# Kernel optimization log

Measured on AMD Instinct MI355X. Metric: run time of the kernel, lower is better.

The kernel has to match this reference:

```python
import jax, jax.numpy as jnp
import numpy as np

B, S, K = 4, 2048, 8
N_NEURONS, N_BASIS, RANK = 64, 32, 8
D_MODEL, D_HID = 256, 1024


def setup_inputs() -> dict:
    key = jax.random.key(0)
    ks = jax.random.split(key, 10)
    x = jax.random.normal(ks[0], (B, S, D_MODEL), dtype=jnp.float32)
    neuron_idx = jax.random.randint(ks[1], (B, S, K), 0, N_NEURONS)
    w = jax.random.uniform(ks[2], (B, S, K), dtype=jnp.float32)
    neuron_weights = w / jnp.sum(w, axis=-1, keepdims=True)  # softmax-like routing weights
    neuron_recipes = jax.random.normal(ks[3], (N_NEURONS, N_BASIS), dtype=jnp.float32) * 0.5
    sc = 0.1
    basis_A1 = jax.random.normal(ks[4], (N_BASIS, 16, RANK, 8), dtype=jnp.float32) * sc
    basis_A2 = jax.random.normal(ks[5], (N_BASIS, RANK, 16, 8), dtype=jnp.float32) * sc
    basis_B1 = jax.random.normal(ks[6], (N_BASIS, 8, RANK, 32), dtype=jnp.float32) * sc
    basis_B2 = jax.random.normal(ks[7], (N_BASIS, RANK, 8, 32), dtype=jnp.float32) * sc
    w_down_w = jax.random.normal(ks[8], (D_HID, D_MODEL), dtype=jnp.float32) * (1.0 / np.sqrt(D_HID))
    w_down_b = jnp.zeros((D_MODEL,), dtype=jnp.float32)
    return {
        "x": x, "neuron_idx": neuron_idx, "neuron_weights": neuron_weights,
        "neuron_recipes": neuron_recipes,
        "basis_A1": basis_A1, "basis_A2": basis_A2,
        "basis_B1": basis_B1, "basis_B2": basis_B2,
        "w_down_w": w_down_w, "w_down_b": w_down_b,
    }


def reference(x, neuron_idx, neuron_weights, neuron_recipes,
              basis_A1, basis_A2, basis_B1, basis_B2, w_down_w, w_down_b):
    Bt, St, D = x.shape
    # --- routing: gather recipes of selected neurons, softmax, weighted-combine ---
    sel = neuron_recipes[neuron_idx]                       # [B,S,k,n_basis]
    sel = jax.nn.softmax(sel, axis=-1)
    wr = jnp.einsum('bskn,bsk->bsn', sel, neuron_weights)  # [B,S,n_basis]
    # --- build per-token TT cores from basis banks (get_neuron_tt_cores) ---
    cA1 = jnp.einsum('bsn,nirk->bsirk', wr, basis_A1)      # [B,S,16,r,8]
    cA2 = jnp.einsum('bsn,nrjl->bsrjl', wr, basis_A2)      # [B,S,r,16,8]
    cB1 = jnp.einsum('bsn,nirk->bsirk', wr, basis_B1)      # [B,S,8,r,32]
    cB2 = jnp.einsum('bsn,nrjl->bsrjl', wr, basis_B2)      # [B,S,r,8,32]
    # --- TT FFN: 256 -> 64 ---
    x_fold = x.reshape(Bt, St, 16, 16)
    temp = jnp.einsum('bsij,bsirk->bsjrk', x_fold, cA1)
    h = jnp.einsum('bsjrk,bsrjl->bskl', temp, cA2).reshape(Bt, St, 64)
    # --- TT FFN: 64 -> 1024 ---
    h_fold = h.reshape(Bt, St, 8, 8)
    temp = jnp.einsum('bsij,bsirk->bsjrk', h_fold, cB1)
    out = jnp.einsum('bsjrk,bsrjl->bskl', temp, cB2).reshape(Bt, St, D_HID)
    out = jax.nn.gelu(out, approximate=False)              # torch F.gelu default = exact erf
    return out @ w_down_w + w_down_b                       # [B,S,256]
```

## Files before the change

### kernel.cpp

```cpp
#include <hip/hip_runtime.h>
#include <math.h>


typedef unsigned short u16;
typedef unsigned int u32;
typedef __attribute__((ext_vector_type(8))) __bf16 bf16x8;
typedef __attribute__((ext_vector_type(4))) float f32x4;
typedef __attribute__((ext_vector_type(16))) float f32x16;
union ABCast { float4 f; bf16x8 v; };
union U4Cast { u32 u[4]; bf16x8 v; };
union BFBits { __bf16 b; u16 u; };
union Pack8 { u16 u[8]; float4 f; };

__device__ __forceinline__ float gelu_exact(float v) {
    return 0.5f * v * (1.0f + erff(v * 0.70710678118654752440f));
}
__device__ __forceinline__ u16 f2bf_bits(float f) { BFBits c; c.b = (__bf16)f; return c.u; }
__device__ __forceinline__ float bfbits2f(u16 u) { BFBits c; c.u = u; return (float)c.b; }

__global__ __launch_bounds__(64) void k_route(
    const int* __restrict__ nidx, const float* __restrict__ nw,
    const float* __restrict__ recipes, float* __restrict__ wr_out,
    u16* __restrict__ wrAh, u16* __restrict__ wrAl)
{
    const int t = blockIdx.x * 64 + threadIdx.x;
    float acc[32];
#pragma unroll
    for (int n = 0; n < 32; n++) acc[n] = 0.f;
#pragma unroll
    for (int k = 0; k < 8; k++) {
        const int   id = nidx[t * 8 + k];
        const float wk = nw[t * 8 + k];
        const float4* row = (const float4*)(recipes + id * 32);
        float v[32];
#pragma unroll
        for (int q = 0; q < 8; q++) {
            float4 f = row[q];
            v[q*4+0] = f.x; v[q*4+1] = f.y; v[q*4+2] = f.z; v[q*4+3] = f.w;
        }
        float m = v[0];
#pragma unroll
        for (int n = 1; n < 32; n++) m = fmaxf(m, v[n]);
        float s = 0.f;
#pragma unroll
        for (int n = 0; n < 32; n++) { float e = expf(v[n] - m); v[n] = e; s += e; }
        const float iv = wk / s;
#pragma unroll
        for (int n = 0; n < 32; n++) acc[n] += v[n] * iv;
    }
    float4* o = (float4*)(wr_out + t * 32);
#pragma unroll
    for (int q = 0; q < 8; q++)
        o[q] = make_float4(acc[q*4+0], acc[q*4+1], acc[q*4+2], acc[q*4+3]);

    const int tg16 = t >> 4, tl = t & 15;
#pragma unroll
    for (int c = 0; c < 4; c++) {
        Pack8 ph, pl;
#pragma unroll
        for (int e = 0; e < 8; e++) {
            const float v = acc[c*8 + e];
            const u16 hb = f2bf_bits(v);
            ph.u[e] = hb;
            pl.u[e] = f2bf_bits(v - bfbits2f(hb));
        }
        const int lane = c * 16 + tl;
        *(float4*)(wrAh + (tg16*64 + lane)*8) = ph.f;
        *(float4*)(wrAl + (tg16*64 + lane)*8) = pl.f;
    }
}

__global__ __launch_bounds__(512) void k_stageA(
    const float* __restrict__ x, const float* __restrict__ wr,
    const float* __restrict__ A1, const float* __restrict__ A2,
    float* __restrict__ h_out)
{
    __shared__ float ca[8 * 1024];
    __shared__ float tl[8 * 1088];
    const int tid = threadIdx.x;
    const int t0  = blockIdx.x * 8;
    {
        const int e2 = tid * 2;
        float2 c[8];
#pragma unroll
        for (int tt = 0; tt < 8; tt++) c[tt] = make_float2(0.f, 0.f);
#pragma unroll 4
        for (int n = 0; n < 32; n++) {
            const float2 a = *(const float2*)(A1 + n * 1024 + e2);
#pragma unroll
            for (int tt = 0; tt < 8; tt++) {
                const float s = wr[(t0 + tt) * 32 + n];
                c[tt].x += s * a.x; c[tt].y += s * a.y;
            }
        }
#pragma unroll
        for (int tt = 0; tt < 8; tt++) *(float2*)(ca + tt * 1024 + e2) = c[tt];
    }
    __syncthreads();
    {
        const int t = tid >> 6, g = tid & 63, j = g >> 2, eh = g & 3;
        float xr[16];
#pragma unroll
        for (int i = 0; i < 16; i++) xr[i] = x[(t0 + t) * 256 + i * 16 + j];
        float tr[16];
#pragma unroll
        for (int q = 0; q < 16; q++) tr[q] = 0.f;
#pragma unroll
        for (int i = 0; i < 16; i++) {
            const float xv = xr[i];
#pragma unroll
            for (int q = 0; q < 4; q++) {
                const float4 cv = *(const float4*)(ca + t * 1024 + i * 64 + eh * 16 + q * 4);
                tr[q*4+0] += xv * cv.x; tr[q*4+1] += xv * cv.y;
                tr[q*4+2] += xv * cv.z; tr[q*4+3] += xv * cv.w;
            }
        }
#pragma unroll
        for (int q = 0; q < 4; q++)
            *(float4*)(tl + t * 1088 + j * 68 + eh * 16 + q * 4) =
                make_float4(tr[q*4+0], tr[q*4+1], tr[q*4+2], tr[q*4+3]);
    }
    __syncthreads();
    {
        const int e2 = tid * 2;
        float2 c[8];
#pragma unroll
        for (int tt = 0; tt < 8; tt++) c[tt] = make_float2(0.f, 0.f);
#pragma unroll 4
        for (int n = 0; n < 32; n++) {
            const float2 a = *(const float2*)(A2 + n * 1024 + e2);
#pragma unroll
            for (int tt = 0; tt < 8; tt++) {
                const float s = wr[(t0 + tt) * 32 + n];
                c[tt].x += s * a.x; c[tt].y += s * a.y;
            }
        }
#pragma unroll
        for (int tt = 0; tt < 8; tt++) *(float2*)(ca + tt * 1024 + e2) = c[tt];
    }
    __syncthreads();
    {
        const int t = tid >> 6, g = tid & 63, k = g >> 3, l = g & 7;
        float acc = 0.f;
#pragma unroll
        for (int j = 0; j < 16; j++) {
#pragma unroll
            for (int r = 0; r < 8; r++) {
                acc += tl[t * 1088 + j * 68 + r * 8 + k] *
                       ca[t * 1024 + r * 128 + j * 8 + l];
            }
        }
        h_out[(t0 + t) * 64 + g] = acc;
    }
}

__global__ __launch_bounds__(256) void k_bsplit(
    const float* __restrict__ B1, const float* __restrict__ B2,
    u16* __restrict__ o1h, u16* __restrict__ o1l,
    u16* __restrict__ o2h, u16* __restrict__ o2l)
{
    const int slot = blockIdx.x * 256 + threadIdx.x;
    const int bank = slot >> 13, r = (slot >> 10) & 7, g = (slot >> 6) & 15, l = slot & 63;
    const int c = l & 15, nb = 8 * (l >> 4);
    const int base = (bank == 0)
        ? ((g >> 1) * 256 + r * 32 + (g & 1) * 16 + c)
        : (r * 256 + (g >> 1) * 32 + (g & 1) * 16 + c);
    const float* S = (bank ? B2 : B1) + base + nb * 2048;
    Pack8 ph, pl;
#pragma unroll
    for (int e = 0; e < 8; e++) {
        const float v = S[e * 2048];
        const u16 hb = f2bf_bits(v);
        ph.u[e] = hb;
        pl.u[e] = f2bf_bits(v - bfbits2f(hb));
    }
    const int d = ((r * 16 + g) * 64 + l) * 8;
    *(float4*)((bank ? o2h : o1h) + d) = ph.f;
    *(float4*)((bank ? o2l : o1l) + d) = pl.f;
}

__global__ __launch_bounds__(256) void k_wsplit(
    const float* __restrict__ W, u16* __restrict__ wfh, u16* __restrict__ wfl)
{
    const int slot = blockIdx.x * 256 + threadIdx.x;
    const int ng = slot >> 11, kc = (slot >> 6) & 31, l = slot & 63;
    const float* S = W + (kc * 32 + 8 * (l >> 4)) * 256 + ng * 16 + (l & 15);
    Pack8 ph, pl;
#pragma unroll
    for (int e = 0; e < 8; e++) {
        const float v = S[e * 256];
        const u16 hb = f2bf_bits(v);
        ph.u[e] = hb;
        pl.u[e] = f2bf_bits(v - bfbits2f(hb));
    }
    const int d = ((ng * 32 + kc) * 64 + l) * 8;
    *(float4*)(wfh + d) = ph.f;
    *(float4*)(wfl + d) = pl.f;
}

__global__ __launch_bounds__(1024, 2) void k_fusedB(
    const float* __restrict__ hin,
    const u16* __restrict__ wrAh, const u16* __restrict__ wrAl,
    const u16* __restrict__ bf1h, const u16* __restrict__ bf1l,
    const u16* __restrict__ bf2h, const u16* __restrict__ bf2l,
    const u16* __restrict__ wfh, const u16* __restrict__ wfl,
    const float* __restrict__ bias, float* __restrict__ y)
{
    __shared__ __align__(16) unsigned char smem[65536];
    float* stg1 = (float*)smem;
    float* stg2 = stg1 + 8192;
    u16* gAh = (u16*)smem;
    u16* gAl = gAh + 16384;

    const int tid = threadIdx.x;
    const int l   = tid & 63;
    const int w   = tid >> 6;
    const int tg  = blockIdx.x;
    const int t0  = tg * 16;
    const int kP  = l & 31;
    const int jh  = l >> 5;

    float hreg[32];
#pragma unroll
    for (int i = 0; i < 8; i++)
#pragma unroll
        for (int jj = 0; jj < 4; jj++)
            hreg[i*4+jj] = hin[(t0 + w) * 64 + i * 8 + jh * 4 + jj];

    ABCast cu;
    cu.f = *(const float4*)(wrAh + (tg * 64 + l) * 8); const bf16x8 wra_h = cu.v;
    cu.f = *(const float4*)(wrAl + (tg * 64 + l) * 8); const bf16x8 wra_l = cu.v;

    const bool isB2 = (w >= 8);
    const u16* bsrc_h = isB2 ? bf2h : bf1h;
    const u16* bsrc_l = isB2 ? bf2l : bf1l;
    float* cstg = isB2 ? stg2 : stg1;
    const int g0 = (w & 7) * 2;

    f32x16 accw = {0.f,0.f,0.f,0.f,0.f,0.f,0.f,0.f,0.f,0.f,0.f,0.f,0.f,0.f,0.f,0.f};
    u32 Afh0=0,Afh1=0,Afh2=0,Afh3=0, Afl0=0,Afl1=0,Afl2=0,Afl3=0;
    u32 Bfh0=0,Bfh1=0,Bfh2=0,Bfh3=0, Bfl0=0,Bfl1=0,Bfl2=0,Bfl3=0;

    float4 pbh0, pbl0, pbh1, pbl1;
#define LOADB(R) { const int rb_=(R)*16;                                        \
    pbh0 = *(const float4*)(bsrc_h + ((rb_+g0+0)*64+l)*8);                      \
    pbl0 = *(const float4*)(bsrc_l + ((rb_+g0+0)*64+l)*8);                      \
    pbh1 = *(const float4*)(bsrc_h + ((rb_+g0+1)*64+l)*8);                      \
    pbl1 = *(const float4*)(bsrc_l + ((rb_+g0+1)*64+l)*8); }
#define BUILD(BSEL) {                                                           \
    ABCast ch_, cl_;                                                            \
    __builtin_amdgcn_s_setprio(1);                                              \
    ch_.f = pbh0; cl_.f = pbl0;                                                 \
    f32x4 cc = {0.f,0.f,0.f,0.f};                                               \
    cc = __builtin_amdgcn_mfma_f32_16x16x32_bf16(wra_h, ch_.v, cc, 0, 0, 0);    \
    cc = __builtin_amdgcn_mfma_f32_16x16x32_bf16(wra_h, cl_.v, cc, 0, 0, 0);    \
    cc = __builtin_amdgcn_mfma_f32_16x16x32_bf16(wra_l, ch_.v, cc, 0, 0, 0);    \
    ch_.f = pbh1; cl_.f = pbl1;                                                 \
    f32x4 cc2 = {0.f,0.f,0.f,0.f};                                              \
    cc2 = __builtin_amdgcn_mfma_f32_16x16x32_bf16(wra_h, ch_.v, cc2, 0, 0, 0);  \
    cc2 = __builtin_amdgcn_mfma_f32_16x16x32_bf16(wra_h, cl_.v, cc2, 0, 0, 0);  \
    cc2 = __builtin_amdgcn_mfma_f32_16x16x32_bf16(wra_l, ch_.v, cc2, 0, 0, 0);  \
    __builtin_amdgcn_s_setprio(0);                                              \
    { const int gg = g0;                                                        \
      float* cd = cstg + (BSEL)*4096 + (gg>>1)*32 + (gg&1)*16 + (l&15);         \
      _Pragma("unroll")                                                         \
      for (int rg = 0; rg < 4; rg++) cd[(4*(l>>4)+rg)*256] = cc[rg]; }          \
    { const int gg = g0 + 1;                                                    \
      float* cd = cstg + (BSEL)*4096 + (gg>>1)*32 + (gg&1)*16 + (l&15);         \
      _Pragma("unroll")                                                         \
      for (int rg = 0; rg < 4; rg++) cd[(4*(l>>4)+rg)*256] = cc2[rg]; } }

    LOADB(0);
    BUILD(0);
    LOADB(1);
    __syncthreads();

#pragma unroll 1
    for (int r = 0; r < 8; r++) {
        if (r < 7) {
            BUILD((r+1)&1);
            if (r < 6) LOADB(r+2);
        }

        {
            const float* c1b = stg1 + (r & 1) * 4096 + w * 256;
            float t0q=0.f, t1q=0.f, t2q=0.f, t3q=0.f;
#pragma unroll
            for (int i = 0; i < 8; i++) {
                const float cv = c1b[i * 32 + kP];
                t0q += hreg[i*4+0] * cv; t1q += hreg[i*4+1] * cv;
                t2q += hreg[i*4+2] * cv; t3q += hreg[i*4+3] * cv;
            }
            const u16 h0 = f2bf_bits(t0q), h1 = f2bf_bits(t1q),
                      h2 = f2bf_bits(t2q), h3 = f2bf_bits(t3q);
            const u16 q0 = f2bf_bits(t0q - bfbits2f(h0)), q1 = f2bf_bits(t1q - bfbits2f(h1)),
                      q2 = f2bf_bits(t2q - bfbits2f(h2)), q3 = f2bf_bits(t3q - bfbits2f(h3));
            const u32 th0 = (u32)h0 | ((u32)h1 << 16), th1 = (u32)h2 | ((u32)h3 << 16);
            const u32 tl0 = (u32)q0 | ((u32)q1 << 16), tl1 = (u32)q2 | ((u32)q3 << 16);
            const u32 ph0 = (u32)__shfl_xor((int)th0, 32);
            const u32 ph1 = (u32)__shfl_xor((int)th1, 32);
            const u32 pl0 = (u32)__shfl_xor((int)tl0, 32);
            const u32 pl1 = (u32)__shfl_xor((int)tl1, 32);
            const u32 a0 = jh ? ph0 : th0, a1 = jh ? ph1 : th1;
            const u32 a2 = jh ? th0 : ph0, a3 = jh ? th1 : ph1;
            const u32 b0 = jh ? pl0 : tl0, b1 = jh ? pl1 : tl1;
            const u32 b2 = jh ? tl0 : pl0, b3 = jh ? tl1 : pl1;
            if ((r & 1) == jh) {
                Afh0 = a0; Afh1 = a1; Afh2 = a2; Afh3 = a3;
                Afl0 = b0; Afl1 = b1; Afl2 = b2; Afl3 = b3;
            }
        }

        {
            const float* c2b = stg2 + (r & 1) * 4096 + w * 256;
            const float v0 = c2b[0*32+kP], v1 = c2b[1*32+kP], v2 = c2b[2*32+kP],
                        v3 = c2b[3*32+kP], v4 = c2b[4*32+kP], v5 = c2b[5*32+kP],
                        v6 = c2b[6*32+kP], v7 = c2b[7*32+kP];
            const u16 e0 = f2bf_bits(v0), e1 = f2bf_bits(v1), e2 = f2bf_bits(v2),
                      e3 = f2bf_bits(v3), e4 = f2bf_bits(v4), e5 = f2bf_bits(v5),
                      e6 = f2bf_bits(v6), e7 = f2bf_bits(v7);
            const u16 f0 = f2bf_bits(v0 - bfbits2f(e0)), f1 = f2bf_bits(v1 - bfbits2f(e1)),
                      f2 = f2bf_bits(v2 - bfbits2f(e2)), f3 = f2bf_bits(v3 - bfbits2f(e3)),
                      f4 = f2bf_bits(v4 - bfbits2f(e4)), f5 = f2bf_bits(v5 - bfbits2f(e5)),
                      f6 = f2bf_bits(v6 - bfbits2f(e6)), f7 = f2bf_bits(v7 - bfbits2f(e7));
            if ((r & 1) == jh) {
                Bfh0 = (u32)e0 | ((u32)e1 << 16); Bfh1 = (u32)e2 | ((u32)e3 << 16);
                Bfh2 = (u32)e4 | ((u32)e5 << 16); Bfh3 = (u32)e6 | ((u32)e7 << 16);
                Bfl0 = (u32)f0 | ((u32)f1 << 16); Bfl1 = (u32)f2 | ((u32)f3 << 16);
                Bfl2 = (u32)f4 | ((u32)f5 << 16); Bfl3 = (u32)f6 | ((u32)f7 << 16);
            }
        }

        if (r & 1) {
            U4Cast ua;
            ua.u[0]=Afh0; ua.u[1]=Afh1; ua.u[2]=Afh2; ua.u[3]=Afh3; const bf16x8 Ah = ua.v;
            ua.u[0]=Afl0; ua.u[1]=Afl1; ua.u[2]=Afl2; ua.u[3]=Afl3; const bf16x8 Al = ua.v;
            ua.u[0]=Bfh0; ua.u[1]=Bfh1; ua.u[2]=Bfh2; ua.u[3]=Bfh3; const bf16x8 Bh = ua.v;
            ua.u[0]=Bfl0; ua.u[1]=Bfl1; ua.u[2]=Bfl2; ua.u[3]=Bfl3; const bf16x8 Bl = ua.v;
            accw = __builtin_amdgcn_mfma_f32_32x32x16_bf16(Ah, Bh, accw, 0, 0, 0);
            accw = __builtin_amdgcn_mfma_f32_32x32x16_bf16(Ah, Bl, accw, 0, 0, 0);
            accw = __builtin_amdgcn_mfma_f32_32x32x16_bf16(Al, Bh, accw, 0, 0, 0);
        }
        __syncthreads();
    }
#undef LOADB
#undef BUILD

    {
#pragma unroll
        for (int rg = 0; rg < 16; rg++) {
            const int k = (rg & 3) + 8 * (rg >> 2) + 4 * jh;
            const float v = gelu_exact(accw[rg]);
            const u16 hbits = f2bf_bits(v);
            const u16 lbits = f2bf_bits(v - bfbits2f(hbits));
            const int idx = (k * 64 + (kP >> 3) * 16 + w) * 8 + (kP & 7);
            gAh[idx] = hbits; gAl[idx] = lbits;
        }
    }
    __syncthreads();

    if (w < 8) {
        f32x4 dacc0 = {0.f,0.f,0.f,0.f}, dacc1 = {0.f,0.f,0.f,0.f};
        const int wb0 = w * 16384 + l * 8;
        const int wb1 = (w + 8) * 16384 + l * 8;
#pragma unroll 2
        for (int kc = 0; kc < 32; kc++) {
            cu.f = *(const float4*)(gAh + (kc * 64 + l) * 8); const bf16x8 ah = cu.v;
            cu.f = *(const float4*)(gAl + (kc * 64 + l) * 8); const bf16x8 al = cu.v;
            ABCast c0, c1, c2, c3;
            c0.f = *(const float4*)(wfh + wb0 + kc * 512); const bf16x8 bh0 = c0.v;
            c1.f = *(const float4*)(wfl + wb0 + kc * 512); const bf16x8 bl0 = c1.v;
            c2.f = *(const float4*)(wfh + wb1 + kc * 512); const bf16x8 bh1 = c2.v;
            c3.f = *(const float4*)(wfl + wb1 + kc * 512); const bf16x8 bl1 = c3.v;
            dacc0 = __builtin_amdgcn_mfma_f32_16x16x32_bf16(ah, bh0, dacc0, 0, 0, 0);
            dacc0 = __builtin_amdgcn_mfma_f32_16x16x32_bf16(ah, bl0, dacc0, 0, 0, 0);
            dacc0 = __builtin_amdgcn_mfma_f32_16x16x32_bf16(al, bh0, dacc0, 0, 0, 0);
            dacc1 = __builtin_amdgcn_mfma_f32_16x16x32_bf16(ah, bh1, dacc1, 0, 0, 0);
            dacc1 = __builtin_amdgcn_mfma_f32_16x16x32_bf16(ah, bl1, dacc1, 0, 0, 0);
            dacc1 = __builtin_amdgcn_mfma_f32_16x16x32_bf16(al, bh1, dacc1, 0, 0, 0);
        }
        const int n0 = w * 16 + (l & 15);
        const int n1 = (w + 8) * 16 + (l & 15);
        const float b0 = bias[n0], b1 = bias[n1];
        const int tb = t0 + 4 * (l >> 4);
#pragma unroll
        for (int rg = 0; rg < 4; rg++) {
            y[(tb + rg) * 256 + n0] = dacc0[rg] + b0;
            y[(tb + rg) * 256 + n1] = dacc1[rg] + b1;
        }
    }
}

extern "C" void kernel_launch(void* const* d_in, const int* in_sizes, int n_in,
                              void* d_out, int out_size, void* d_ws, size_t ws_size,
                              hipStream_t stream)
{
    const float* x    = (const float*)d_in[0];
    const int*   nidx = (const int*)  d_in[1];
    const float* nw   = (const float*)d_in[2];
    const float* rec  = (const float*)d_in[3];
    const float* A1   = (const float*)d_in[4];
    const float* A2   = (const float*)d_in[5];
    const float* B1   = (const float*)d_in[6];
    const float* B2   = (const float*)d_in[7];
    const float* Wd   = (const float*)d_in[8];
    const float* bd   = (const float*)d_in[9];
    float* y  = (float*)d_out;

    float* wr  = (float*)d_ws;
    float* h   = wr + 8192 * 32;
    u16* wrAh  = (u16*)(h + 8192 * 64);
    u16* wrAl  = wrAh + 262144;
    u16* b1h   = wrAl + 262144;
    u16* b1l   = b1h + 65536;
    u16* b2h   = b1l + 65536;
    u16* b2l   = b2h + 65536;
    u16* wfh   = b2l + 65536;
    u16* wfl   = wfh + 262144;

    k_route <<<128,  64,   0, stream>>>(nidx, nw, rec, wr, wrAh, wrAl);
    k_stageA<<<1024, 512,  0, stream>>>(x, wr, A1, A2, h);
    k_bsplit<<<64,   256,  0, stream>>>(B1, B2, b1h, b1l, b2h, b2l);
    k_wsplit<<<128,  256,  0, stream>>>(Wd, wfh, wfl);
    k_fusedB<<<512,  1024, 0, stream>>>(h, wrAh, wrAl, b1h, b1l, b2h, b2l, wfh, wfl, bd, y);
}
```

Measured before the change: 98.28 us.

## Transpose stageA LDS layouts, merge weight-split kernels, spread down-proj over all waves

Stores the stage-A intermediate and A2 core in LDS with the rank index innermost, so the final contraction can use float4 loads instead of scalar strided loads. Merges the B-bank and W-down bf16 split kernels into one launch to save a kernel launch. In the fused kernel, the down-projection now runs one 16-column tile per wave across all 16 waves instead of two tiles on 8 waves, to raise parallelism. The new scalar transposed LDS stores may cause bank conflicts.

Result: slower. 109.8 us (+11.8%).

```diff
diff --git a/kernel.cpp b/kernel.cpp
--- a/kernel.cpp
+++ b/kernel.cpp
@@ -116,13 +116,15 @@
             }
         }
 #pragma unroll
-        for (int q = 0; q < 4; q++)
-            *(float4*)(tl + t * 1088 + j * 68 + eh * 16 + q * 4) =
-                make_float4(tr[q*4+0], tr[q*4+1], tr[q*4+2], tr[q*4+3]);
+        for (int q = 0; q < 16; q++) {
+            const int rk = eh * 16 + q, r = rk >> 3, k = rk & 7;
+            tl[t * 1088 + k * 136 + j * 8 + r] = tr[q];
+        }
     }
     __syncthreads();
     {
         const int e2 = tid * 2;
+        const int r = e2 >> 7, j = (e2 >> 3) & 15, l = e2 & 7;
         float2 c[8];
 #pragma unroll
         for (int tt = 0; tt < 8; tt++) c[tt] = make_float2(0.f, 0.f);
@@ -136,7 +138,10 @@
             }
         }
 #pragma unroll
-        for (int tt = 0; tt < 8; tt++) *(float2*)(ca + tt * 1024 + e2) = c[tt];
+        for (int tt = 0; tt < 8; tt++) {
+            ca[tt * 1024 + j * 64 + l * 8 + r]       = c[tt].x;
+            ca[tt * 1024 + j * 64 + (l + 1) * 8 + r] = c[tt].y;
+        }
     }
     __syncthreads();
     {
@@ -145,57 +150,57 @@
 #pragma unroll
         for (int j = 0; j < 16; j++) {
 #pragma unroll
-            for (int r = 0; r < 8; r++) {
-                acc += tl[t * 1088 + j * 68 + r * 8 + k] *
-                       ca[t * 1024 + r * 128 + j * 8 + l];
+            for (int rq = 0; rq < 2; rq++) {
+                const float4 a = *(const float4*)(tl + t * 1088 + k * 136 + j * 8 + rq * 4);
+                const float4 b = *(const float4*)(ca + t * 1024 + j * 64 + l * 8 + rq * 4);
+                acc += a.x * b.x + a.y * b.y + a.z * b.z + a.w * b.w;
             }
         }
         h_out[(t0 + t) * 64 + g] = acc;
     }
 }
 
-__global__ __launch_bounds__(256) void k_bsplit(
+__global__ __launch_bounds__(256) void k_prep(
     const float* __restrict__ B1, const float* __restrict__ B2,
     u16* __restrict__ o1h, u16* __restrict__ o1l,
-    u16* __restrict__ o2h, u16* __restrict__ o2l)
-{
-    const int slot = blockIdx.x * 256 + threadIdx.x;
-    const int bank = slot >> 13, r = (slot >> 10) & 7, g = (slot >> 6) & 15, l = slot & 63;
-    const int c = l & 15, nb = 8 * (l >> 4);
-    const int base = (bank == 0)
-        ? ((g >> 1) * 256 + r * 32 + (g & 1) * 16 + c)
-        : (r * 256 + (g >> 1) * 32 + (g & 1) * 16 + c);
-    const float* S = (bank ? B2 : B1) + base + nb * 2048;
-    Pack8 ph, pl;
-#pragma unroll
-    for (int e = 0; e < 8; e++) {
-        const float v = S[e * 2048];
-        const u16 hb = f2bf_bits(v);
-        ph.u[e] = hb;
-        pl.u[e] = f2bf_bits(v - bfbits2f(hb));
-    }
-    const int d = ((r * 16 + g) * 64 + l) * 8;
-    *(float4*)((bank ? o2h : o1h) + d) = ph.f;
-    *(float4*)((bank ? o2l : o1l) + d) = pl.f;
-}
-
-__global__ __launch_bounds__(256) void k_wsplit(
+    u16* __restrict__ o2h, u16* __restrict__ o2l,
     const float* __restrict__ W, u16* __restrict__ wfh, u16* __restrict__ wfl)
 {
-    const int slot = blockIdx.x * 256 + threadIdx.x;
-    const int ng = slot >> 11, kc = (slot >> 6) & 31, l = slot & 63;
-    const float* S = W + (kc * 32 + 8 * (l >> 4)) * 256 + ng * 16 + (l & 15);
-    Pack8 ph, pl;
-#pragma unroll
-    for (int e = 0; e < 8; e++) {
-        const float v = S[e * 256];
-        const u16 hb = f2bf_bits(v);
-        ph.u[e] = hb;
-        pl.u[e] = f2bf_bits(v - bfbits2f(hb));
-    }
-    const int d = ((ng * 32 + kc) * 64 + l) * 8;
-    *(float4*)(wfh + d) = ph.f;
-    *(float4*)(wfl + d) = pl.f;
+    if (blockIdx.x < 64) {
+        const int slot = blockIdx.x * 256 + threadIdx.x;
+        const int bank = slot >> 13, r = (slot >> 10) & 7, g = (slot >> 6) & 15, l = slot & 63;
+        const int c = l & 15, nb = 8 * (l >> 4);
+        const int base = (bank == 0)
+            ? ((g >> 1) * 256 + r * 32 + (g & 1) * 16 + c)
+            : (r * 256 + (g >> 1) * 32 + (g & 1) * 16 + c);
+        const float* S = (bank ? B2 : B1) + base + nb * 2048;
+        Pack8 ph, pl;
+#pragma unroll
+        for (int e = 0; e < 8; e++) {
+            const float v = S[e * 2048];
+            const u16 hb = f2bf_bits(v);
+            ph.u[e] = hb;
+            pl.u[e] = f2bf_bits(v - bfbits2f(hb));
+        }
+        const int d = ((r * 16 + g) * 64 + l) * 8;
+        *(float4*)((bank ? o2h : o1h) + d) = ph.f;
+        *(float4*)((bank ? o2l : o1l) + d) = pl.f;
+    } else {
+        const int slot = (blockIdx.x - 64) * 256 + threadIdx.x;
+        const int ng = slot >> 11, kc = (slot >> 6) & 31, l = slot & 63;
+        const float* S = W + (kc * 32 + 8 * (l >> 4)) * 256 + ng * 16 + (l & 15);
+        Pack8 ph, pl;
+#pragma unroll
+        for (int e = 0; e < 8; e++) {
+            const float v = S[e * 256];
+            const u16 hb = f2bf_bits(v);
+            ph.u[e] = hb;
+            pl.u[e] = f2bf_bits(v - bfbits2f(hb));
+        }
+        const int d = ((ng * 32 + kc) * 64 + l) * 8;
+        *(float4*)(wfh + d) = ph.f;
+        *(float4*)(wfl + d) = pl.f;
+    }
 }
 
 __global__ __launch_bounds__(1024, 2) void k_fusedB(
@@ -359,35 +364,26 @@
     }
     __syncthreads();
 
-    if (w < 8) {
-        f32x4 dacc0 = {0.f,0.f,0.f,0.f}, dacc1 = {0.f,0.f,0.f,0.f};
-        const int wb0 = w * 16384 + l * 8;
-        const int wb1 = (w + 8) * 16384 + l * 8;
+    {
+        f32x4 dacc = {0.f,0.f,0.f,0.f};
+        const int wb = w * 16384 + l * 8;
 #pragma unroll 2
         for (int kc = 0; kc < 32; kc++) {
             cu.f = *(const float4*)(gAh + (kc * 64 + l) * 8); const bf16x8 ah = cu.v;
             cu.f = *(const float4*)(gAl + (kc * 64 + l) * 8); const bf16x8 al = cu.v;
-            ABCast c0, c1, c2, c3;
-            c0.f = *(const float4*)(wfh + wb0 + kc * 512); const bf16x8 bh0 = c0.v;
-            c1.f = *(const float4*)(wfl + wb0 + kc * 512); const bf16x8 bl0 = c1.v;
-            c2.f = *(const float4*)(wfh + wb1 + kc * 512); const bf16x8 bh1 = c2.v;
-            c3.f = *(const float4*)(wfl + wb1 + kc * 512); const bf16x8 bl1 = c3.v;
-            dacc0 = __builtin_amdgcn_mfma_f32_16x16x32_bf16(ah, bh0, dacc0, 0, 0, 0);
-            dacc0 = __builtin_amdgcn_mfma_f32_16x16x32_bf16(ah, bl0, dacc0, 0, 0, 0);
-            dacc0 = __builtin_amdgcn_mfma_f32_16x16x32_bf16(al, bh0, dacc0, 0, 0, 0);
-            dacc1 = __builtin_amdgcn_mfma_f32_16x16x32_bf16(ah, bh1, dacc1, 0, 0, 0);
-            dacc1 = __builtin_amdgcn_mfma_f32_16x16x32_bf16(ah, bl1, dacc1, 0, 0, 0);
-            dacc1 = __builtin_amdgcn_mfma_f32_16x16x32_bf16(al, bh1, dacc1, 0, 0, 0);
+            ABCast c0, c1;
+            c0.f = *(const float4*)(wfh + wb + kc * 512); const bf16x8 bh = c0.v;
+            c1.f = *(const float4*)(wfl + wb + kc * 512); const bf16x8 bl = c1.v;
+            dacc = __builtin_amdgcn_mfma_f32_16x16x32_bf16(ah, bh, dacc, 0, 0, 0);
+            dacc = __builtin_amdgcn_mfma_f32_16x16x32_bf16(ah, bl, dacc, 0, 0, 0);
+            dacc = __builtin_amdgcn_mfma_f32_16x16x32_bf16(al, bh, dacc, 0, 0, 0);
         }
         const int n0 = w * 16 + (l & 15);
-        const int n1 = (w + 8) * 16 + (l & 15);
-        const float b0 = bias[n0], b1 = bias[n1];
+        const float b0 = bias[n0];
         const int tb = t0 + 4 * (l >> 4);
 #pragma unroll
-        for (int rg = 0; rg < 4; rg++) {
-            y[(tb + rg) * 256 + n0] = dacc0[rg] + b0;
-            y[(tb + rg) * 256 + n1] = dacc1[rg] + b1;
-        }
+        for (int rg = 0; rg < 4; rg++)
+            y[(tb + rg) * 256 + n0] = dacc[rg] + b0;
     }
 }
 
@@ -419,8 +415,7 @@
     u16* wfl   = wfh + 262144;
 
     k_route <<<128,  64,   0, stream>>>(nidx, nw, rec, wr, wrAh, wrAl);
+    k_prep  <<<192,  256,  0, stream>>>(B1, B2, b1h, b1l, b2h, b2l, Wd, wfh, wfl);
     k_stageA<<<1024, 512,  0, stream>>>(x, wr, A1, A2, h);
-    k_bsplit<<<64,   256,  0, stream>>>(B1, B2, b1h, b1l, b2h, b2l);
-    k_wsplit<<<128,  256,  0, stream>>>(Wd, wfh, wfl);
     k_fusedB<<<512,  1024, 0, stream>>>(h, wrAh, wrAl, b1h, b1l, b2h, b2l, wfh, wfl, bd, y);
 }
```
